# Optimization experiments

Measured on AMD Instinct MI355X. Metric: run time of the kernel, lower is better.

## Reference

```python
import jax, jax.numpy as jnp
import numpy as np

D_MODEL = 1024
N_HEADS = 16
HEAD_DIM = D_MODEL // N_HEADS
D_C = 128
THETA = 10000.0


def rope_cos_sin(timestamps):
    # timestamps: (B, L) -> cos, sin: (B, L, HEAD_DIM)
    freqs = 1.0 / (THETA ** (jnp.arange(0, HEAD_DIM, 2, dtype=jnp.float32) / HEAD_DIM))
    t = timestamps[..., None] * freqs            # (B, L, HEAD_DIM//2)
    emb = jnp.concatenate([t, t], axis=-1)       # (B, L, HEAD_DIM)
    return jnp.cos(emb), jnp.sin(emb)


def rotate_half(x):
    x1, x2 = jnp.split(x, 2, axis=-1)
    return jnp.concatenate([-x2, x1], axis=-1)


def setup_inputs() -> dict:
    key = jax.random.key(0)
    ks = jax.random.split(key, 10)
    B, L = 2, 2048
    s = 0.02
    return {
        "query": jax.random.normal(ks[0], (B, L, D_MODEL), jnp.float32),
        "timestamps_q": jax.random.uniform(ks[1], (B, L), jnp.float32) * 365.0,
        "timestamps_kv": jax.random.uniform(ks[2], (B, L), jnp.float32) * 365.0,
        "w_kv_c": jax.random.normal(ks[3], (D_MODEL, D_C), jnp.float32) * s,
        "w_kc_up": jax.random.normal(ks[4], (D_C, D_MODEL), jnp.float32) * s,
        "w_vc_up": jax.random.normal(ks[5], (D_C, D_MODEL), jnp.float32) * s,
        "w_qr": jax.random.normal(ks[6], (D_MODEL, D_MODEL), jnp.float32) * s,
        "w_kr": jax.random.normal(ks[7], (D_MODEL, D_MODEL), jnp.float32) * s,
        "w_o": jax.random.normal(ks[8], (D_MODEL, D_MODEL), jnp.float32) * s,
    }


def reference(query, timestamps_q, timestamps_kv, w_kv_c, w_kc_up, w_vc_up, w_qr, w_kr, w_o):
    B, Lq, _ = query.shape
    key_value = query  # self-attention path (key_value defaults to query)
    Lk = key_value.shape[1]

    def heads(x, L):  # (B, L, D) -> (B, H, L, hd)
        return x.reshape(B, L, N_HEADS, HEAD_DIM).transpose(0, 2, 1, 3)

    c_kv = key_value @ w_kv_c                      # (B, Lk, d_c) low-rank KV
    k_c = heads(c_kv @ w_kc_up, Lk)
    v_c = heads(c_kv @ w_vc_up, Lk)
    q_r = heads(query @ w_qr, Lq)
    k_r = heads(key_value @ w_kr, Lk)

    cos_q, _ = rope_cos_sin(timestamps_q)
    cos_k, _ = rope_cos_sin(timestamps_kv)
    cos_q = cos_q[:, None]                          # (B, 1, Lq, hd)
    cos_k = cos_k[:, None]                          # (B, 1, Lk, hd)
    # Faithful to original (which passes cos_k in the `sin` slot):
    q_r = q_r * cos_q + rotate_half(q_r) * cos_k
    k_r = k_r * cos_q + rotate_half(k_r) * cos_k

    scale = HEAD_DIM ** -0.5
    qs = q_r * scale
    attn = jnp.einsum("bhqd,bhkd->bhqk", qs, k_c) + jnp.einsum("bhqd,bhkd->bhqk", qs, k_r)
    attn_weights = jax.nn.softmax(attn, axis=-1)
    out = jnp.einsum("bhqk,bhkd->bhqd", attn_weights, v_c)
    out = out.transpose(0, 2, 1, 3).reshape(B, Lq, D_MODEL)
    return out @ w_o
```

## Files before the change

### kernel.cpp

```cpp
#include <hip/hip_runtime.h>

typedef float          f32x4    __attribute__((ext_vector_type(4)));
typedef float          f32x2    __attribute__((ext_vector_type(2)));
typedef float          float8v  __attribute__((ext_vector_type(8)));
typedef unsigned short ushort8v __attribute__((ext_vector_type(8)));
typedef __bf16         bf16x8   __attribute__((ext_vector_type(8)));

__device__ __forceinline__ unsigned short f2b(float x) {
  union { __bf16 b; unsigned short u; } v;
  v.b = (__bf16)x;
  return v.u;
}
__device__ __forceinline__ float b2f(unsigned short h) {
  union { unsigned u; float f; } v; v.u = ((unsigned)h) << 16;
  return v.f;
}

__device__ __forceinline__ void g2lds16(const unsigned short* g,
                                        unsigned short* l) {
  __builtin_amdgcn_global_load_lds(
      (const __attribute__((address_space(1))) unsigned int*)g,
      (__attribute__((address_space(3))) unsigned int*)l, 16, 0, 0);
}

__global__ __launch_bounds__(256) void prep_kernel(
    const float* __restrict__ X, unsigned short* __restrict__ Xb, int cvtb,
    int n8,
    const float* __restrict__ w0, unsigned short* __restrict__ t0,
    const float* __restrict__ w1, unsigned short* __restrict__ t1,
    const float* __restrict__ w2, unsigned short* __restrict__ t2,
    const float* __restrict__ w3, unsigned short* __restrict__ t3,
    const float* __restrict__ w4, unsigned short* __restrict__ t4,
    const float* __restrict__ w5, unsigned short* __restrict__ t5,
    const float* __restrict__ tq, const float* __restrict__ tk,
    f32x2* __restrict__ ctab) {
  __shared__ unsigned short T[64 * 72];
  const int tid = threadIdx.x;
  int blk = blockIdx.x;
  if (blk < cvtb) {
    int i = blk * 256 + tid;
    if (i >= n8) return;
    float8v v = reinterpret_cast<const float8v*>(X)[i];
    ushort8v h;
#pragma unroll
    for (int j = 0; j < 8; ++j) h[j] = f2b(v[j]);
    reinterpret_cast<ushort8v*>(Xb)[i] = h;
    return;
  }
  blk -= cvtb;
  if (blk >= 864) {
    int idx = (blk - 864) * 256 + tid;
    int row = idx >> 5, i = idx & 31;
    float f = exp2f(-(float)i * (13.287712379549449f / 32.f));
    f32x2 c;
    c[0] = cosf(tq[row] * f);
    c[1] = cosf(tk[row] * f);
    ctab[idx] = c;
    return;
  }
  const float* W; unsigned short* WT; int K, N, bx, by;
  if (blk < 256)      { W = w0; WT = t0; K = 1024; N = 1024; bx = blk & 15;         by = blk >> 4; }
  else if (blk < 512) { W = w1; WT = t1; K = 1024; N = 1024; bx = (blk - 256) & 15; by = (blk - 256) >> 4; }
  else if (blk < 544) { W = w2; WT = t2; K = 1024; N = 128;  bx = (blk - 512) & 1;  by = (blk - 512) >> 1; }
  else if (blk < 576) { W = w3; WT = t3; K = 128;  N = 1024; bx = (blk - 544) & 15; by = (blk - 544) >> 4; }
  else if (blk < 608) { W = w4; WT = t4; K = 128;  N = 1024; bx = (blk - 576) & 15; by = (blk - 576) >> 4; }
  else                { W = w5; WT = t5; K = 1024; N = 1024; bx = (blk - 608) & 15; by = (blk - 608) >> 4; }
  const int n0 = bx * 64, k0 = by * 64;
#pragma unroll
  for (int it = 0; it < 2; ++it) {
    int c = tid + it * 256;
    int r = c >> 3, cc = c & 7;
    float8v v = *reinterpret_cast<const float8v*>(
        &W[(size_t)(k0 + r) * N + n0 + cc * 8]);
    ushort8v h;
#pragma unroll
    for (int j = 0; j < 8; ++j) h[j] = f2b(v[j]);
    *reinterpret_cast<ushort8v*>(&T[r * 72 + cc * 8]) = h;
  }
  __syncthreads();
#pragma unroll
  for (int it = 0; it < 2; ++it) {
    int c = tid + it * 256;
    int n = c >> 3, kc = c & 7;
    ushort8v y;
#pragma unroll
    for (int j = 0; j < 8; ++j) y[j] = T[(kc * 8 + j) * 72 + n];
    *reinterpret_cast<ushort8v*>(&WT[(size_t)(n0 + n) * K + k0 + kc * 8]) = y;
  }
}

template <int TM, typename CT, bool ACC>
__global__ __launch_bounds__(256) void gemm_bt(
    const unsigned short* __restrict__ A, const unsigned short* __restrict__ Bt,
    CT* __restrict__ C, int M, int N, int K) {
  __shared__ unsigned short As[TM * 64];
  __shared__ unsigned short Bs[128 * 64];
  const int tid = threadIdx.x;
  const int m0 = blockIdx.y * TM, n0 = blockIdx.x * 128;
  const int wave = tid >> 6, lane = tid & 63;
  const int wm = (wave >> 1) * (TM / 2), wn = (wave & 1) * 64;
  const int l16 = lane & 15, quad = lane >> 4;
  constexpr int MI = TM / 32;

  f32x4 acc[MI][4];
#pragma unroll
  for (int i = 0; i < MI; ++i)
#pragma unroll
    for (int j = 0; j < 4; ++j)
#pragma unroll
      for (int r = 0; r < 4; ++r) acc[i][j][r] = 0.f;

  for (int k0 = 0; k0 < K; k0 += 64) {
    __syncthreads();
#pragma unroll
    for (int it = 0; it < TM * 8 / 256; ++it) {
      int c = it * 256 + tid;
      int m = c >> 3, kc = (c & 7) ^ (m & 7);
      g2lds16(&A[(size_t)(m0 + m) * K + k0 + kc * 8], &As[c * 8]);
    }
#pragma unroll
    for (int it = 0; it < 4; ++it) {
      int c = it * 256 + tid;
      int n = c >> 3, kc = (c & 7) ^ (n & 7);
      g2lds16(&Bt[(size_t)(n0 + n) * K + k0 + kc * 8], &Bs[c * 8]);
    }
    __syncthreads();

#pragma unroll
    for (int ks = 0; ks < 2; ++ks) {
      bf16x8 af[MI], bfr[4];
#pragma unroll
      for (int mi = 0; mi < MI; ++mi) {
        int m = wm + mi * 16 + l16;
        af[mi] = *reinterpret_cast<const bf16x8*>(
            &As[(m * 8 + ((ks * 4 + quad) ^ (m & 7))) * 8]);
      }
#pragma unroll
      for (int ni = 0; ni < 4; ++ni) {
        int n = wn + ni * 16 + l16;
        bfr[ni] = *reinterpret_cast<const bf16x8*>(
            &Bs[(n * 8 + ((ks * 4 + quad) ^ (n & 7))) * 8]);
      }
#pragma unroll
      for (int mi = 0; mi < MI; ++mi)
#pragma unroll
        for (int ni = 0; ni < 4; ++ni)
          acc[mi][ni] = __builtin_amdgcn_mfma_f32_16x16x32_bf16(
              af[mi], bfr[ni], acc[mi][ni], 0, 0, 0);
    }
  }

#pragma unroll
  for (int mi = 0; mi < MI; ++mi)
#pragma unroll
    for (int ni = 0; ni < 4; ++ni) {
      int row = m0 + wm + mi * 16 + quad * 4;
      int col = n0 + wn + ni * 16 + l16;
#pragma unroll
      for (int r = 0; r < 4; ++r) {
        size_t idx = (size_t)(row + r) * N + col;
        float val = acc[mi][ni][r];
        if constexpr (sizeof(CT) == 2) {
          if constexpr (ACC) val += b2f(C[idx]);
          C[idx] = f2b(val);
        } else {
          if constexpr (ACC) val += C[idx];
          C[idx] = val;
        }
      }
    }
}

__global__ __launch_bounds__(256) void gemm_fused3(
    const unsigned short* __restrict__ A, const unsigned short* __restrict__ Bt,
    unsigned short* __restrict__ Cq, unsigned short* __restrict__ Ck,
    unsigned short* __restrict__ Cc, const f32x2* __restrict__ ctab, int K) {
  __shared__ unsigned short As[1024 * 8];
  __shared__ unsigned short Bs[1024 * 8];
  const int tid = threadIdx.x;
  const int m0 = blockIdx.y * 128, n0 = blockIdx.x * 128;
  const int wave = tid >> 6, lane = tid & 63;
  const int wm = (wave >> 1) * 64, wn = (wave & 1) * 64;
  const int l16 = lane & 15, quad = lane >> 4;

  f32x4 acc[4][4];
#pragma unroll
  for (int i = 0; i < 4; ++i)
#pragma unroll
    for (int j = 0; j < 4; ++j)
#pragma unroll
      for (int r = 0; r < 4; ++r) acc[i][j][r] = 0.f;

  for (int k0 = 0; k0 < K; k0 += 64) {
    __syncthreads();
#pragma unroll
    for (int it = 0; it < 4; ++it) {
      int c = it * 256 + tid;
      int m = c >> 3, kc = (c & 7) ^ (m & 7);
      g2lds16(&A[(size_t)(m0 + m) * K + k0 + kc * 8], &As[c * 8]);
    }
#pragma unroll
    for (int it = 0; it < 4; ++it) {
      int c = it * 256 + tid;
      int n = c >> 3, kc = (c & 7) ^ (n & 7);
      g2lds16(&Bt[(size_t)(n0 + n) * K + k0 + kc * 8], &Bs[c * 8]);
    }
    __syncthreads();

#pragma unroll
    for (int ks = 0; ks < 2; ++ks) {
      bf16x8 af[4], bfr[4];
#pragma unroll
      for (int mi = 0; mi < 4; ++mi) {
        int m = wm + mi * 16 + l16;
        af[mi] = *reinterpret_cast<const bf16x8*>(
            &As[(m * 8 + ((ks * 4 + quad) ^ (m & 7))) * 8]);
      }
#pragma unroll
      for (int ni = 0; ni < 4; ++ni) {
        int n = wn + ni * 16 + l16;
        bfr[ni] = *reinterpret_cast<const bf16x8*>(
            &Bs[(n * 8 + ((ks * 4 + quad) ^ (n & 7))) * 8]);
      }
#pragma unroll
      for (int mi = 0; mi < 4; ++mi)
#pragma unroll
        for (int ni = 0; ni < 4; ++ni)
          acc[mi][ni] = __builtin_amdgcn_mfma_f32_16x16x32_bf16(
              af[mi], bfr[ni], acc[mi][ni], 0, 0, 0);
    }
  }

  if (n0 < 2048) {
    const bool isq = (n0 < 1024);
    unsigned short* dst = isq ? Cq : Ck;
    const int cb = isq ? 0 : 1024;
    const float s = isq ? 0.18033688011112042f : 1.0f;
#pragma unroll
    for (int mi = 0; mi < 4; ++mi)
#pragma unroll
      for (int r = 0; r < 4; ++r) {
        int row = m0 + wm + mi * 16 + quad * 4 + r;
        const f32x2* crow = &ctab[(size_t)row * 32];
#pragma unroll
        for (int np = 0; np < 2; ++np) {
          f32x2 cc = crow[np * 16 + l16];
          float v1 = acc[mi][np][r], v2 = acc[mi][np + 2][r];
          int col = n0 - cb + wn + np * 16 + l16;
          dst[(size_t)row * 1024 + col]      = f2b((v1 * cc[0] - v2 * cc[1]) * s);
          dst[(size_t)row * 1024 + col + 32] = f2b((v2 * cc[0] + v1 * cc[1]) * s);
        }
      }
  } else {
#pragma unroll
    for (int mi = 0; mi < 4; ++mi)
#pragma unroll
      for (int ni = 0; ni < 4; ++ni) {
        int row = m0 + wm + mi * 16 + quad * 4;
        int col = n0 - 2048 + wn + ni * 16 + l16;
#pragma unroll
        for (int r = 0; r < 4; ++r)
          Cc[(size_t)(row + r) * 128 + col] = f2b(acc[mi][ni][r]);
      }
  }
}

__global__ __launch_bounds__(256) void gemm_fused2(
    const unsigned short* __restrict__ A, const unsigned short* __restrict__ Bt,
    unsigned short* __restrict__ Ck, unsigned short* __restrict__ Cv, int K) {
  __shared__ unsigned short As[1024 * 8];
  __shared__ unsigned short Bs[1024 * 8];
  const int tid = threadIdx.x;
  const int m0 = blockIdx.y * 128, n0 = blockIdx.x * 128;
  const int wave = tid >> 6, lane = tid & 63;
  const int wm = (wave >> 1) * 64, wn = (wave & 1) * 64;
  const int l16 = lane & 15, quad = lane >> 4;

  f32x4 acc[4][4];
#pragma unroll
  for (int i = 0; i < 4; ++i)
#pragma unroll
    for (int j = 0; j < 4; ++j)
#pragma unroll
      for (int r = 0; r < 4; ++r) acc[i][j][r] = 0.f;

  for (int k0 = 0; k0 < K; k0 += 64) {
    __syncthreads();
#pragma unroll
    for (int it = 0; it < 4; ++it) {
      int c = it * 256 + tid;
      int m = c >> 3, kc = (c & 7) ^ (m & 7);
      g2lds16(&A[(size_t)(m0 + m) * K + k0 + kc * 8], &As[c * 8]);
    }
#pragma unroll
    for (int it = 0; it < 4; ++it) {
      int c = it * 256 + tid;
      int n = c >> 3, kc = (c & 7) ^ (n & 7);
      g2lds16(&Bt[(size_t)(n0 + n) * K + k0 + kc * 8], &Bs[c * 8]);
    }
    __syncthreads();

#pragma unroll
    for (int ks = 0; ks < 2; ++ks) {
      bf16x8 af[4], bfr[4];
#pragma unroll
      for (int mi = 0; mi < 4; ++mi) {
        int m = wm + mi * 16 + l16;
        af[mi] = *reinterpret_cast<const bf16x8*>(
            &As[(m * 8 + ((ks * 4 + quad) ^ (m & 7))) * 8]);
      }
#pragma unroll
      for (int ni = 0; ni < 4; ++ni) {
        int n = wn + ni * 16 + l16;
        bfr[ni] = *reinterpret_cast<const bf16x8*>(
            &Bs[(n * 8 + ((ks * 4 + quad) ^ (n & 7))) * 8]);
      }
#pragma unroll
      for (int mi = 0; mi < 4; ++mi)
#pragma unroll
        for (int ni = 0; ni < 4; ++ni)
          acc[mi][ni] = __builtin_amdgcn_mfma_f32_16x16x32_bf16(
              af[mi], bfr[ni], acc[mi][ni], 0, 0, 0);
    }
  }

  const bool first = (n0 < 1024);
  unsigned short* dst = first ? Ck : Cv;
  int cb = first ? 0 : 1024;
#pragma unroll
  for (int mi = 0; mi < 4; ++mi)
#pragma unroll
    for (int ni = 0; ni < 4; ++ni) {
      int row = m0 + wm + mi * 16 + quad * 4;
      int col = n0 - cb + wn + ni * 16 + l16;
#pragma unroll
      for (int r = 0; r < 4; ++r) {
        size_t idx = (size_t)(row + r) * 1024 + col;
        float val = acc[mi][ni][r];
        if (first) val += b2f(dst[idx]);
        dst[idx] = f2b(val);
      }
    }
}

__global__ __launch_bounds__(256) void vtrans_kernel(
    const unsigned short* __restrict__ v, unsigned short* __restrict__ vt,
    int L) {
  __shared__ unsigned short T[64 * 72];
  const int tid = threadIdx.x;
  const int l0 = blockIdx.x * 64, bh = blockIdx.y;
  const size_t inbase = ((size_t)(bh >> 4) * L) * 1024 + (bh & 15) * 64;
  const size_t outbase = (size_t)bh * 64 * L;
#pragma unroll
  for (int it = 0; it < 2; ++it) {
    int c = tid + it * 256;
    int l = c >> 3, dc = c & 7;
    ushort8v x = *reinterpret_cast<const ushort8v*>(
        &v[inbase + (size_t)(l0 + l) * 1024 + dc * 8]);
    *reinterpret_cast<ushort8v*>(&T[l * 72 + dc * 8]) = x;
  }
  __syncthreads();
#pragma unroll
  for (int it = 0; it < 2; ++it) {
    int c = tid + it * 256;
    int d = c >> 3, g = c & 7;
    ushort8v y;
#pragma unroll
    for (int e = 0; e < 8; ++e) {
      int k = ((g >> 2) << 5) | ((e >> 2) << 4) | (((g >> 1) & 1) << 3) |
              ((g & 1) << 2) | (e & 3);
      y[e] = T[k * 72 + d];
    }
    *reinterpret_cast<ushort8v*>(&vt[outbase + (size_t)d * L + l0 + g * 8]) = y;
  }
}

__global__ __launch_bounds__(512) void flash15_kernel(
    const unsigned short* __restrict__ qs, const unsigned short* __restrict__ ks,
    const unsigned short* __restrict__ vt, unsigned short* __restrict__ o,
    int L) {
  __shared__ unsigned short KV[2][2][2][512 * 8];
  const int tid = threadIdx.x;
  const int wave = tid >> 6, lane = tid & 63;
  const int half = wave >> 2;
  const int l16 = lane & 15, quad = lane >> 4;
  const int bh = blockIdx.y;
  const int qb = blockIdx.x * 128 + (wave & 3) * 32;
  const size_t base = ((size_t)(bh >> 4) * L) * 1024 + (bh & 15) * 64;
  const size_t vtbase = (size_t)bh * 64 * L;
  const int kvoff = half * (L >> 1);
  const int sid = tid & 255;

  bf16x8 aq[2][2];
#pragma unroll
  for (int mt = 0; mt < 2; ++mt) {
    size_t qrow = base + (size_t)(qb + mt * 16 + l16) * 1024;
    aq[mt][0] = *reinterpret_cast<const bf16x8*>(&qs[qrow + quad * 8]);
    aq[mt][1] = *reinterpret_cast<const bf16x8*>(&qs[qrow + 32 + quad * 8]);
  }

  ushort8v onesu;
#pragma unroll
  for (int j = 0; j < 8; ++j) onesu[j] = 0x3F80;
  bf16x8 ones = *reinterpret_cast<bf16x8*>(&onesu);

  f32x4 oacc[2][4];
  f32x4 lacc[2];
#pragma unroll
  for (int mt = 0; mt < 2; ++mt) {
#pragma unroll
    for (int r = 0; r < 4; ++r) lacc[mt][r] = 0.f;
#pragma unroll
    for (int nt = 0; nt < 4; ++nt)
#pragma unroll
      for (int r = 0; r < 4; ++r) oacc[mt][nt][r] = 0.f;
  }

  const int T = L / 128;
#pragma unroll
  for (int it = 0; it < 2; ++it) {
    int c = it * 256 + sid;
    int key = c >> 3, dc = (c & 7) ^ (key & 7);
    g2lds16(&ks[base + (size_t)(kvoff + key) * 1024 + dc * 8],
            &KV[0][half][0][c * 8]);
  }
#pragma unroll
  for (int it = 0; it < 2; ++it) {
    int c = it * 256 + sid;
    int d = c >> 3, kc = (c & 7) ^ (d & 7);
    g2lds16(&vt[vtbase + (size_t)d * L + kvoff + kc * 8],
            &KV[1][half][0][c * 8]);
  }

  for (int t = 0; t < T; ++t) {
    __syncthreads();
    if (t + 1 < T) {
      int k0 = kvoff + (t + 1) * 64, nb = (t + 1) & 1;
#pragma unroll
      for (int it = 0; it < 2; ++it) {
        int c = it * 256 + sid;
        int key = c >> 3, dc = (c & 7) ^ (key & 7);
        g2lds16(&ks[base + (size_t)(k0 + key) * 1024 + dc * 8],
                &KV[0][half][nb][c * 8]);
      }
#pragma unroll
      for (int it = 0; it < 2; ++it) {
        int c = it * 256 + sid;
        int d = c >> 3, kc = (c & 7) ^ (d & 7);
        g2lds16(&vt[vtbase + (size_t)d * L + k0 + kc * 8],
                &KV[1][half][nb][c * 8]);
      }
    }
    const int cb = t & 1;
    const unsigned short* Ks = &KV[0][half][cb][0];
    const unsigned short* Vs = &KV[1][half][cb][0];

    f32x4 st[2][4];
#pragma unroll
    for (int nt = 0; nt < 4; ++nt) {
      int key = nt * 16 + l16;
      int dc0 = quad ^ (key & 7);
      int dc1 = (4 + quad) ^ (key & 7);
      bf16x8 bk0 = *reinterpret_cast<const bf16x8*>(&Ks[(key * 8 + dc0) * 8]);
      bf16x8 bk1 = *reinterpret_cast<const bf16x8*>(&Ks[(key * 8 + dc1) * 8]);
#pragma unroll
      for (int mt = 0; mt < 2; ++mt) {
        f32x4 z; z[0] = z[1] = z[2] = z[3] = 0.f;
        z = __builtin_amdgcn_mfma_f32_16x16x32_bf16(bk0, aq[mt][0], z, 0, 0, 0);
        z = __builtin_amdgcn_mfma_f32_16x16x32_bf16(bk1, aq[mt][1], z, 0, 0, 0);
        st[mt][nt] = z;
      }
    }

    bf16x8 ap[2][2];
#pragma unroll
    for (int mt = 0; mt < 2; ++mt) {
#pragma unroll
      for (int hf = 0; hf < 2; ++hf)
#pragma unroll
        for (int w = 0; w < 4; ++w) {
          int nt = 2 * hf + (w >> 1), p = w & 1;
          ap[mt][hf][2 * w] =
              (__bf16)__builtin_amdgcn_exp2f(st[mt][nt][2 * p]);
          ap[mt][hf][2 * w + 1] =
              (__bf16)__builtin_amdgcn_exp2f(st[mt][nt][2 * p + 1]);
        }
      lacc[mt] = __builtin_amdgcn_mfma_f32_16x16x32_bf16(ap[mt][0], ones,
                                                         lacc[mt], 0, 0, 0);
      lacc[mt] = __builtin_amdgcn_mfma_f32_16x16x32_bf16(ap[mt][1], ones,
                                                         lacc[mt], 0, 0, 0);
    }

#pragma unroll
    for (int nt = 0; nt < 4; ++nt) {
      int d = nt * 16 + l16;
#pragma unroll
      for (int hf = 0; hf < 2; ++hf) {
        int kc = (hf * 4 + quad) ^ (d & 7);
        bf16x8 bv = *reinterpret_cast<const bf16x8*>(&Vs[(d * 8 + kc) * 8]);
#pragma unroll
        for (int mt = 0; mt < 2; ++mt)
          oacc[mt][nt] = __builtin_amdgcn_mfma_f32_16x16x32_bf16(
              ap[mt][hf], bv, oacc[mt][nt], 0, 0, 0);
      }
    }
  }

  __syncthreads();
  float* cbuf = (float*)&KV[0][0][0][0];
  if (half == 1) {
    int slot = ((wave - 4) * 64 + lane) * 44;
#pragma unroll
    for (int mt = 0; mt < 2; ++mt) {
#pragma unroll
      for (int nt = 0; nt < 4; ++nt)
        *reinterpret_cast<f32x4*>(&cbuf[slot + (mt * 4 + nt) * 4]) =
            oacc[mt][nt];
      *reinterpret_cast<f32x4*>(&cbuf[slot + 32 + mt * 4]) = lacc[mt];
    }
  }
  __syncthreads();
  if (half == 0) {
    int slot = (wave * 64 + lane) * 44;
#pragma unroll
    for (int mt = 0; mt < 2; ++mt) {
#pragma unroll
      for (int nt = 0; nt < 4; ++nt) {
        f32x4 ov = *reinterpret_cast<const f32x4*>(
            &cbuf[slot + (mt * 4 + nt) * 4]);
#pragma unroll
        for (int r = 0; r < 4; ++r) oacc[mt][nt][r] += ov[r];
      }
      f32x4 lv = *reinterpret_cast<const f32x4*>(&cbuf[slot + 32 + mt * 4]);
#pragma unroll
      for (int r = 0; r < 4; ++r) lacc[mt][r] += lv[r];
    }
#pragma unroll
    for (int mt = 0; mt < 2; ++mt)
#pragma unroll
      for (int r = 0; r < 4; ++r) {
        float inv = __builtin_amdgcn_rcpf(lacc[mt][r]);
        int q = qb + mt * 16 + quad * 4 + r;
#pragma unroll
        for (int nt = 0; nt < 4; ++nt)
          o[base + (size_t)q * 1024 + nt * 16 + l16] =
              f2b(oacc[mt][nt][r] * inv);
      }
  }
}

extern "C" void kernel_launch(void* const* d_in, const int* in_sizes, int n_in,
                              void* d_out, int out_size, void* d_ws, size_t ws_size,
                              hipStream_t stream) {
  const float* X    = (const float*)d_in[0];
  const float* tq   = (const float*)d_in[1];
  const float* tk   = (const float*)d_in[2];
  const float* wkvc = (const float*)d_in[3];
  const float* wkc  = (const float*)d_in[4];
  const float* wvc  = (const float*)d_in[5];
  const float* wqr  = (const float*)d_in[6];
  const float* wkr  = (const float*)d_in[7];
  const float* wo   = (const float*)d_in[8];

  const int D = 1024, DC = 128, L = 2048;
  const int M = in_sizes[0] / D;
  const int B = M / L;
  const int NBH = B * 16;
  (void)n_in; (void)out_size; (void)ws_size;

  unsigned short* p = (unsigned short*)d_ws;
  auto take = [&](size_t n) { unsigned short* r = p; p += n; return r; };
  unsigned short* Xb    = take((size_t)M * D);
  unsigned short* qsb   = take((size_t)M * D);
  unsigned short* ksb   = take((size_t)M * D);
  unsigned short* vcb   = take((size_t)M * D);
  unsigned short* ckv   = take((size_t)M * DC);
  unsigned short* Wbig  = take((size_t)(2 * D + DC) * D);
  unsigned short* Wkcvc = take((size_t)(2 * D) * DC);
  unsigned short* WoT   = take((size_t)D * D);
  f32x2* ctab = (f32x2*)take((size_t)M * 32 * 4);
  unsigned short* vtb   = Xb;
  unsigned short* obuf  = vcb;

  const int n8 = M * D / 8;
  const int cvtb = (n8 + 255) / 256;
  const int ropeb = M / 8;
  prep_kernel<<<cvtb + 864 + ropeb, 256, 0, stream>>>(
      X, Xb, cvtb, n8,
      wqr,  Wbig,
      wkr,  Wbig + (size_t)D * D,
      wkvc, Wbig + (size_t)2 * D * D,
      wkc,  Wkcvc,
      wvc,  Wkcvc + (size_t)D * DC,
      wo,   WoT,
      tq, tk, ctab);

  {
    dim3 g((2 * D + DC) / 128, M / 128);
    gemm_fused3<<<g, 256, 0, stream>>>(Xb, Wbig, qsb, ksb, ckv, ctab, D);
  }
  {
    dim3 g(2 * D / 128, M / 128);
    gemm_fused2<<<g, 256, 0, stream>>>(ckv, Wkcvc, ksb, vcb, DC);
  }

  dim3 tg(L / 64, NBH);
  vtrans_kernel<<<tg, 256, 0, stream>>>(vcb, vtb, L);

  dim3 fg(L / 128, NBH);
  flash15_kernel<<<fg, 512, 0, stream>>>(qsb, ksb, vtb, obuf, L);

  {
    dim3 g(D / 128, M / 64);
    gemm_bt<64, float, false><<<g, 256, 0, stream>>>(
        obuf, WoT, (float*)d_out, M, D, D);
  }
}
```

Baseline: 218.5 us.

## Fuse V transpose into up-projection epilogue and swizzle GEMM block order for XCDs

```diff
diff --git a/kernel.cpp b/kernel.cpp
--- a/kernel.cpp
+++ b/kernel.cpp
@@ -4,6 +4,7 @@
 typedef float          f32x2    __attribute__((ext_vector_type(2)));
 typedef float          float8v  __attribute__((ext_vector_type(8)));
 typedef unsigned short ushort8v __attribute__((ext_vector_type(8)));
+typedef unsigned short ushort4v __attribute__((ext_vector_type(4)));
 typedef __bf16         bf16x8   __attribute__((ext_vector_type(8)));
 
 __device__ __forceinline__ unsigned short f2b(float x) {
@@ -96,7 +97,10 @@
   __shared__ unsigned short As[TM * 64];
   __shared__ unsigned short Bs[128 * 64];
   const int tid = threadIdx.x;
-  const int m0 = blockIdx.y * TM, n0 = blockIdx.x * 128;
+  const int id = blockIdx.x, cpx = gridDim.x >> 3;
+  const int swz = (id & 7) * cpx + (id >> 3);
+  const int nwx = N / 128;
+  const int m0 = (swz / nwx) * TM, n0 = (swz % nwx) * 128;
   const int wave = tid >> 6, lane = tid & 63;
   const int wm = (wave >> 1) * (TM / 2), wn = (wave & 1) * 64;
   const int l16 = lane & 15, quad = lane >> 4;
@@ -178,7 +182,9 @@
   __shared__ unsigned short As[1024 * 8];
   __shared__ unsigned short Bs[1024 * 8];
   const int tid = threadIdx.x;
-  const int m0 = blockIdx.y * 128, n0 = blockIdx.x * 128;
+  const int id = blockIdx.x;
+  const int swz = (id & 7) * 68 + (id >> 3);
+  const int m0 = (swz / 17) * 128, n0 = (swz % 17) * 128;
   const int wave = tid >> 6, lane = tid & 63;
   const int wm = (wave >> 1) * 64, wn = (wave & 1) * 64;
   const int l16 = lane & 15, quad = lane >> 4;
@@ -267,7 +273,7 @@
 
 __global__ __launch_bounds__(256) void gemm_fused2(
     const unsigned short* __restrict__ A, const unsigned short* __restrict__ Bt,
-    unsigned short* __restrict__ Ck, unsigned short* __restrict__ Cv, int K) {
+    unsigned short* __restrict__ Ck, unsigned short* __restrict__ vt, int K) {
   __shared__ unsigned short As[1024 * 8];
   __shared__ unsigned short Bs[1024 * 8];
   const int tid = threadIdx.x;
@@ -324,54 +330,38 @@
     }
   }
 
-  const bool first = (n0 < 1024);
-  unsigned short* dst = first ? Ck : Cv;
-  int cb = first ? 0 : 1024;
-#pragma unroll
-  for (int mi = 0; mi < 4; ++mi)
-#pragma unroll
-    for (int ni = 0; ni < 4; ++ni) {
-      int row = m0 + wm + mi * 16 + quad * 4;
-      int col = n0 - cb + wn + ni * 16 + l16;
-#pragma unroll
-      for (int r = 0; r < 4; ++r) {
-        size_t idx = (size_t)(row + r) * 1024 + col;
-        float val = acc[mi][ni][r];
-        if (first) val += b2f(dst[idx]);
-        dst[idx] = f2b(val);
-      }
-    }
-}
-
-__global__ __launch_bounds__(256) void vtrans_kernel(
-    const unsigned short* __restrict__ v, unsigned short* __restrict__ vt,
-    int L) {
-  __shared__ unsigned short T[64 * 72];
-  const int tid = threadIdx.x;
-  const int l0 = blockIdx.x * 64, bh = blockIdx.y;
-  const size_t inbase = ((size_t)(bh >> 4) * L) * 1024 + (bh & 15) * 64;
-  const size_t outbase = (size_t)bh * 64 * L;
-#pragma unroll
-  for (int it = 0; it < 2; ++it) {
-    int c = tid + it * 256;
-    int l = c >> 3, dc = c & 7;
-    ushort8v x = *reinterpret_cast<const ushort8v*>(
-        &v[inbase + (size_t)(l0 + l) * 1024 + dc * 8]);
-    *reinterpret_cast<ushort8v*>(&T[l * 72 + dc * 8]) = x;
-  }
-  __syncthreads();
-#pragma unroll
-  for (int it = 0; it < 2; ++it) {
-    int c = tid + it * 256;
-    int d = c >> 3, g = c & 7;
-    ushort8v y;
-#pragma unroll
-    for (int e = 0; e < 8; ++e) {
-      int k = ((g >> 2) << 5) | ((e >> 2) << 4) | (((g >> 1) & 1) << 3) |
-              ((g & 1) << 2) | (e & 3);
-      y[e] = T[k * 72 + d];
-    }
-    *reinterpret_cast<ushort8v*>(&vt[outbase + (size_t)d * L + l0 + g * 8]) = y;
+  if (n0 < 1024) {
+#pragma unroll
+    for (int mi = 0; mi < 4; ++mi)
+#pragma unroll
+      for (int ni = 0; ni < 4; ++ni) {
+        int row = m0 + wm + mi * 16 + quad * 4;
+        int col = n0 + wn + ni * 16 + l16;
+#pragma unroll
+        for (int r = 0; r < 4; ++r) {
+          size_t idx = (size_t)(row + r) * 1024 + col;
+          Ck[idx] = f2b(acc[mi][ni][r] + b2f(Ck[idx]));
+        }
+      }
+  } else {
+    const int L = 2048;
+#pragma unroll
+    for (int mi = 0; mi < 4; ++mi)
+#pragma unroll
+      for (int ni = 0; ni < 4; ++ni) {
+        int row = m0 + wm + mi * 16 + quad * 4;
+        int col = n0 - 1024 + wn + ni * 16 + l16;
+        int l = row & (L - 1);
+        int bh = ((row >> 11) << 4) | (col >> 6);
+        int d = col & 63;
+        int s = (l & ~63) | (((l >> 5) & 1) << 5) | (((l >> 3) & 1) << 4) |
+                (((l >> 2) & 1) << 3) | (((l >> 4) & 1) << 2);
+        ushort4v w;
+#pragma unroll
+        for (int r = 0; r < 4; ++r) w[r] = f2b(acc[mi][ni][r]);
+        *reinterpret_cast<ushort4v*>(
+            &vt[(size_t)bh * 64 * L + (size_t)d * L + s]) = w;
+      }
   }
 }
 
@@ -596,23 +586,19 @@
       tq, tk, ctab);
 
   {
-    dim3 g((2 * D + DC) / 128, M / 128);
-    gemm_fused3<<<g, 256, 0, stream>>>(Xb, Wbig, qsb, ksb, ckv, ctab, D);
+    gemm_fused3<<<(2 * D + DC) / 128 * (M / 128), 256, 0, stream>>>(
+        Xb, Wbig, qsb, ksb, ckv, ctab, D);
   }
   {
     dim3 g(2 * D / 128, M / 128);
-    gemm_fused2<<<g, 256, 0, stream>>>(ckv, Wkcvc, ksb, vcb, DC);
-  }
-
-  dim3 tg(L / 64, NBH);
-  vtrans_kernel<<<tg, 256, 0, stream>>>(vcb, vtb, L);
+    gemm_fused2<<<g, 256, 0, stream>>>(ckv, Wkcvc, ksb, vtb, DC);
+  }
 
   dim3 fg(L / 128, NBH);
   flash15_kernel<<<fg, 512, 0, stream>>>(qsb, ksb, vtb, obuf, L);
 
   {
-    dim3 g(D / 128, M / 64);
-    gemm_bt<64, float, false><<<g, 256, 0, stream>>>(
+    gemm_bt<64, float, false><<<(D / 128) * (M / 64), 256, 0, stream>>>(
         obuf, WoT, (float*)d_out, M, D, D);
   }
 }
```

New measurement: 199.4 us. 1.1x faster.
